# Kernel tuning notes

Measured on AMD Instinct MI355X. Metric: run time of the kernel, lower is better.

## Reference

```python
import jax, jax.numpy as jnp
import numpy as np

B, TIN, E, TOUT, NMEL = 32, 512, 576, 400, 80
PRE, ARNN, DRNN, ADIM, NF, KS = 256, 1024, 1024, 128, 32, 31


def setup_inputs() -> dict:
    key = jax.random.key(0)
    ks = jax.random.split(key, 24)
    r = lambda i, sh, s=0.02: jax.random.normal(ks[i], sh, dtype=jnp.float32) * s
    return {
        'memory': jax.random.normal(ks[0], (B, TIN, E), dtype=jnp.float32) * 0.5,
        'decoder_inputs': jax.random.normal(ks[1], (B, TOUT, NMEL), dtype=jnp.float32) * 0.5,
        'prenet_W1': r(2, (PRE, NMEL)),
        'prenet_W2': r(3, (PRE, PRE)),
        'att_Wih': r(4, (4 * ARNN, PRE + E)),
        'att_Whh': r(5, (4 * ARNN, ARNN)),
        'att_bih': r(6, (4 * ARNN,)),
        'att_bhh': r(7, (4 * ARNN,)),
        'qW': r(8, (ADIM, ARNN)),
        'memW': r(9, (ADIM, E)),
        'convW': r(10, (NF, 2, KS)),
        'convb': r(11, (NF,)),
        'locW': r(12, (ADIM, NF)),
        'vW': r(13, (ADIM,)),
        'dec_Wih': r(14, (4 * DRNN, ARNN + E)),
        'dec_Whh': r(15, (4 * DRNN, DRNN)),
        'dec_bih': r(16, (4 * DRNN,)),
        'dec_bhh': r(17, (4 * DRNN,)),
        'projW': r(18, (NMEL, DRNN + E)),
        'projb': r(19, (NMEL,)),
        'gateW': r(20, (1, DRNN + E)),
        'gateb': r(21, (1,)),
        'memory_lengths': jnp.clip(jax.random.randint(ks[22], (B,), 1, TIN + 1), 16, TIN),
    }


def _lstm(x, h, c, Wih, Whh, bih, bhh):
    g = x @ Wih.T + bih + h @ Whh.T + bhh
    i, f, gg, o = jnp.split(g, 4, axis=-1)  # torch LSTMCell gate order i,f,g,o
    c = jax.nn.sigmoid(f) * c + jax.nn.sigmoid(i) * jnp.tanh(gg)
    h = jax.nn.sigmoid(o) * jnp.tanh(c)
    return h, c


def _forward(memory, decoder_inputs, prenet_W1, prenet_W2, att_Wih, att_Whh, att_bih,
             att_bhh, qW, memW, convW, convb, locW, vW, dec_Wih, dec_Whh, dec_bih,
             dec_bhh, projW, projb, gateW, gateb, memory_lengths):
    b, tin, e = memory.shape
    # go frame + teacher forcing inputs -> prenet (dropout off in deterministic eval)
    go = jnp.zeros((b, 1, NMEL), dtype=memory.dtype)
    di = jnp.concatenate([go, decoder_inputs], axis=1)          # [B, T+1, NMEL]
    x = jax.nn.relu(di @ prenet_W1.T)
    x = jax.nn.relu(x @ prenet_W2.T)                            # [B, T+1, PRE]
    xs = jnp.swapaxes(x, 0, 1)[:-1]                             # [T, B, PRE]
    pmem = memory @ memW.T                                      # [B, TIN, ADIM]
    invalid = jnp.arange(tin)[None, :] >= memory_lengths[:, None]
    pad = KS // 2

    init = (jnp.zeros((b, ARNN)), jnp.zeros((b, ARNN)),
            jnp.zeros((b, DRNN)), jnp.zeros((b, DRNN)),
            jnp.zeros((b, tin)), jnp.zeros((b, tin)),
            jnp.zeros((b, e)))

    def step(carry, xt):
        ah, ac, dh, dc, aw, awc, ctx = carry
        ci = jnp.concatenate([xt, ctx], axis=-1)
        ah, ac = _lstm(ci, ah, ac, att_Wih, att_Whh, att_bih, att_bhh)
        ah = ac  # faithful to source: dropout(attention_cell) overwrites hidden (identity in eval)
        wc = jnp.stack([aw, awc], axis=1)                       # [B, 2, TIN]
        loc = jax.lax.conv_general_dilated(
            wc, convW, (1,), [(pad, pad)],
            dimension_numbers=('NCH', 'OIH', 'NCH')) + convb[None, :, None]
        loc = jnp.swapaxes(loc, 1, 2) @ locW.T                  # [B, TIN, ADIM]
        q = (ah @ qW.T)[:, None, :]                             # [B, 1, ADIM]
        en = jnp.tanh(q + pmem + loc) @ vW                      # [B, TIN]
        en = jnp.where(invalid, -jnp.inf, en)
        aw = jax.nn.softmax(en, axis=1)
        ctx = jnp.einsum('bt,bte->be', aw, memory)
        awc = awc + aw
        d_in = jnp.concatenate([ah, ctx], axis=-1)
        dh, dc = _lstm(d_in, dh, dc, dec_Wih, dec_Whh, dec_bih, dec_bhh)
        dhc = jnp.concatenate([dh, ctx], axis=-1)
        mel = dhc @ projW.T + projb                             # [B, NMEL]
        gate = (dhc @ gateW.T + gateb)[:, 0]                    # [B]
        return (ah, ac, dh, dc, aw, awc, ctx), (mel, gate, aw)

    _, (mels, gates, aligns) = jax.lax.scan(step, init, xs)
    mel_out = jnp.swapaxes(jnp.swapaxes(mels, 0, 1), 1, 2)      # [B, NMEL, T]
    gate_out = jnp.swapaxes(gates, 0, 1)                        # [B, T]
    align_out = jnp.swapaxes(aligns, 0, 1)                      # [B, T, TIN]
    return mel_out, gate_out, align_out


def reference(memory, decoder_inputs, prenet_W1, prenet_W2, att_Wih, att_Whh, att_bih,
              att_bhh, qW, memW, convW, convb, locW, vW, dec_Wih, dec_Whh, dec_bih,
              dec_bhh, projW, projb, gateW, gateb, memory_lengths):
    return _forward(memory, decoder_inputs, prenet_W1, prenet_W2, att_Wih, att_Whh,
                    att_bih, att_bhh, qW, memW, convW, convb, locW, vW, dec_Wih,
                    dec_Whh, dec_bih, dec_bhh, projW, projb, gateW, gateb,
                    memory_lengths)
```

## Files before the change

kernel.cpp:

```cpp
#include <hip/hip_runtime.h>
#include <stdint.h>


#define NB  32
#define TI  512
#define ED  576
#define TO  400
#define NM  80
#define PR  256
#define AR  1024
#define DR  1024
#define AD  128
#define NFl 32
#define KSz 31
#define KA  1856
#define KD  2624
#define NG  4096
#define NKT_A 58
#define NKT_D 82
#define REL_IDX 320
#define MF_OFF  512

#define LDS_WA_BYTES (NKT_A*512*2)
#define LDS_WD_BYTES (NKT_D*512*2)
#define LDS_SCR_FLOATS 4352
#define LDS_TOTAL (LDS_WA_BYTES + LDS_WD_BYTES + LDS_SCR_FLOATS*4)

typedef __attribute__((ext_vector_type(8))) short bf8_t;
typedef __attribute__((ext_vector_type(4))) float f4_t;
typedef __attribute__((ext_vector_type(2))) float f2_t;
typedef unsigned long long ull;

__device__ __forceinline__ short f2bf(float f){
  union { float f; unsigned u; } v; v.f = f;
  unsigned r = v.u + 0x7fffu + ((v.u >> 16) & 1u);
  return (short)(r >> 16);
}
__device__ __forceinline__ float bf2f(short s){
  union { unsigned u; float f; } v; v.u = ((unsigned)(unsigned short)s) << 16; return v.f;
}
__device__ __forceinline__ float sigm(float x){ return 1.f / (1.f + __expf(-x)); }

__device__ __forceinline__ f4_t MFMA(bf8_t a, bf8_t b, f4_t c){
  return __builtin_amdgcn_mfma_f32_16x16x32_bf16(a, b, c, 0, 0, 0);
}

__device__ __forceinline__ float cld(const float* p){
  return __hip_atomic_load(p, __ATOMIC_RELAXED, __HIP_MEMORY_SCOPE_AGENT);
}
__device__ __forceinline__ void cst(float* p, float v){
  __hip_atomic_store(p, v, __ATOMIC_RELAXED, __HIP_MEMORY_SCOPE_AGENT);
}
__device__ __forceinline__ ull cld8(const void* p){
  return __hip_atomic_load((const ull*)p, __ATOMIC_RELAXED, __HIP_MEMORY_SCOPE_AGENT);
}
__device__ __forceinline__ void cst8(void* p, ull v){
  __hip_atomic_store((ull*)p, v, __ATOMIC_RELAXED, __HIP_MEMORY_SCOPE_AGENT);
}
__device__ __forceinline__ bf8_t cld_bf8(const short* p){
  union { bf8_t v; ull q[2]; } u;
  u.q[0] = cld8(p); u.q[1] = cld8(p + 4);
  return u.v;
}
__device__ __forceinline__ void cst_bf8(short* p, bf8_t v){
  union { bf8_t v; ull q[2]; } u; u.v = v;
  cst8(p, u.q[0]); cst8(p + 4, u.q[1]);
}

__device__ __forceinline__ bf8_t packrow(const float* p){
  f4_t a = *(const f4_t*)p;
  f4_t b = *(const f4_t*)(p + 4);
  bf8_t r;
  r[0]=f2bf(a[0]); r[1]=f2bf(a[1]); r[2]=f2bf(a[2]); r[3]=f2bf(a[3]);
  r[4]=f2bf(b[0]); r[5]=f2bf(b[1]); r[6]=f2bf(b[2]); r[7]=f2bf(b[3]);
  return r;
}
__device__ __forceinline__ bf8_t packrow_coh(const float* p){
  union { ull q; float f[2]; } u0, u1, u2, u3;
  u0.q = cld8(p); u1.q = cld8(p + 2); u2.q = cld8(p + 4); u3.q = cld8(p + 6);
  bf8_t r;
  r[0]=f2bf(u0.f[0]); r[1]=f2bf(u0.f[1]);
  r[2]=f2bf(u1.f[0]); r[3]=f2bf(u1.f[1]);
  r[4]=f2bf(u2.f[0]); r[5]=f2bf(u2.f[1]);
  r[6]=f2bf(u3.f[0]); r[7]=f2bf(u3.f[1]);
  return r;
}

struct Par {
  const float *X2, *PMEM;
  const short *WA, *WD, *WQ, *WLOC, *MEMBT, *PJW;
  const float *BSA, *BSD;
  const float *convW, *convb, *vW;
  const float *projb, *gateb;
  const int *mlen;
  float *SBUF, *GATT, *GDEC, *AC, *DH, *DC, *CTX, *AW, *AWC, *EN, *QP;
  short *ABA, *ABD;
  float *out_mel, *out_gate, *out_align;
  unsigned *FLAGS;
};

__device__ __forceinline__ const float* aptr_att(const Par& p, int rp, int t, int b, int k){
  if (k < PR)      return p.X2 + ((size_t)t*NB + b)*PR + k;
  if (k < PR+ED)   return p.CTX + (size_t)rp*NB*ED + b*ED + (k - PR);
  return p.AC + (size_t)rp*NB*AR + b*AR + (k - PR - ED);
}

__device__ __forceinline__ void loadD(const Par& p, int cpar, int ks, int lane,
                                      bf8_t& a0, bf8_t& a1){
  if (ks >= 32 && ks < 50){
    const int kb = ks*32 + ((lane >> 4) << 3);
    const float* c0 = p.CTX + (size_t)cpar*NB*ED + (size_t)(lane & 15)*ED + (kb - AR);
    const float* c1 = p.CTX + (size_t)cpar*NB*ED + (size_t)(16 + (lane & 15))*ED + (kb - AR);
    a0 = packrow_coh(c0);
    a1 = packrow_coh(c1);
  } else {
    a0 = cld_bf8(p.ABD + ((size_t)(0*NKT_D + ks)*64 + lane)*8);
    a1 = cld_bf8(p.ABD + ((size_t)(1*NKT_D + ks)*64 + lane)*8);
  }
}

__device__ __forceinline__ void gbar(unsigned* flags, unsigned tgt){
  __syncthreads();
  if (threadIdx.x == 0)
    __hip_atomic_store(&flags[blockIdx.x], tgt, __ATOMIC_RELAXED, __HIP_MEMORY_SCOPE_AGENT);
  if (blockIdx.x == 0){
    if (threadIdx.x < 256){
      while (__hip_atomic_load(&flags[threadIdx.x], __ATOMIC_RELAXED, __HIP_MEMORY_SCOPE_AGENT) < tgt) {}
    }
    __syncthreads();
    if (threadIdx.x == 0)
      __hip_atomic_store(&flags[REL_IDX], tgt, __ATOMIC_RELAXED, __HIP_MEMORY_SCOPE_AGENT);
  }
  if (threadIdx.x == 0){
    while (__hip_atomic_load(&flags[REL_IDX], __ATOMIC_RELAXED, __HIP_MEMORY_SCOPE_AGENT) < tgt) {}
  }
  __syncthreads();
}

__device__ __forceinline__ void sibbar(unsigned* mf, int bid, int tid, unsigned tgt){
  __syncthreads();
  if (tid == 0)
    __hip_atomic_store(&mf[bid], tgt, __ATOMIC_RELAXED, __HIP_MEMORY_SCOPE_AGENT);
  const int g = (bid >> 3) << 3;
  if (tid < 8){
    while (__hip_atomic_load(&mf[g + tid], __ATOMIC_RELAXED, __HIP_MEMORY_SCOPE_AGENT) < tgt) {}
  }
  __syncthreads();
}

__device__ __forceinline__ void reduce8(float* scr, f4_t& a0, f4_t& a1, int lane, int wv){
  if (wv > 0){
    float* slot = scr + (size_t)((wv - 1)*64 + lane)*8;
    *(f4_t*)slot       = a0;
    *(f4_t*)(slot + 4) = a1;
  }
  __syncthreads();
  if (wv == 0){
    #pragma unroll
    for (int w = 0; w < 7; ++w){
      const float* s2 = scr + (size_t)(w*64 + lane)*8;
      a0 += *(const f4_t*)s2;
      a1 += *(const f4_t*)(s2 + 4);
    }
  }
  __syncthreads();
}

__device__ __forceinline__ void dec_gemm(const Par& p, const short* sWD, float* scr,
                                         int cpar, int bid, int lane, int wv){
  f4_t acc0 = (f4_t){0.f,0.f,0.f,0.f}, acc1 = (f4_t){0.f,0.f,0.f,0.f};
  {
    bf8_t A0[6], A1[6];
    #pragma unroll
    for (int i = 0; i < 6; ++i) loadD(p, cpar, wv + i*8, lane, A0[i], A1[i]);
    #pragma unroll
    for (int i = 0; i < 6; ++i){
      const bf8_t bw = *((const bf8_t*)sWD + (wv + i*8)*64 + lane);
      acc0 = MFMA(A0[i], bw, acc0);
      acc1 = MFMA(A1[i], bw, acc1);
    }
  }
  {
    bf8_t A0[5], A1[5];
    #pragma unroll
    for (int i = 0; i < 5; ++i){
      const int ks = wv + (i + 6)*8;
      if (ks < NKT_D) loadD(p, cpar, ks, lane, A0[i], A1[i]);
    }
    #pragma unroll
    for (int i = 0; i < 5; ++i){
      const int ks = wv + (i + 6)*8;
      if (ks < NKT_D){
        const bf8_t bw = *((const bf8_t*)sWD + ks*64 + lane);
        acc0 = MFMA(A0[i], bw, acc0);
        acc1 = MFMA(A1[i], bw, acc1);
      }
    }
  }
  reduce8(scr, acc0, acc1, lane, wv);
  if (wv == 0){
    const int col = lane & 15, rb2 = (lane >> 4) << 2;
    const int jp = (col & 3)*1024 + bid*4 + (col >> 2);
    const float bs = p.BSD[jp];
    #pragma unroll
    for (int r = 0; r < 4; ++r){
      cst(&p.GDEC[(size_t)(rb2 + r)*NG + jp],      acc0[r] + bs);
      cst(&p.GDEC[(size_t)(16 + rb2 + r)*NG + jp], acc1[r] + bs);
    }
  }
}

__device__ void dec_out(const Par& p, int b, int tprev, int tid, float* sIN){
  const float* ctxg = p.CTX + (size_t)(tprev & 1)*NB*ED + b*ED;
  float cx0 = cld(ctxg + tid);
  float cx1 = (tid < ED - 512) ? cld(ctxg + 512 + tid) : 0.f;
  const int u0 = tid, u1 = tid + 512;
  float g0i = cld(&p.GDEC[b*NG + u0]);
  float g0f = cld(&p.GDEC[b*NG + 1024 + u0]);
  float g0g = cld(&p.GDEC[b*NG + 2048 + u0]);
  float g0o = cld(&p.GDEC[b*NG + 3072 + u0]);
  float g1i = cld(&p.GDEC[b*NG + u1]);
  float g1f = cld(&p.GDEC[b*NG + 1024 + u1]);
  float g1g = cld(&p.GDEC[b*NG + 2048 + u1]);
  float g1o = cld(&p.GDEC[b*NG + 3072 + u1]);
  float dc0 = p.DC[b*DR + u0];
  float dc1 = p.DC[b*DR + u1];
  sIN[1024 + tid] = cx0;
  if (tid < ED - 512) sIN[1024 + 512 + tid] = cx1;
  if (tid < 448) sIN[1600 + tid] = 0.f;
  {
    float c0 = sigm(g0f) * dc0 + sigm(g0i) * tanhf(g0g);
    float c1 = sigm(g1f) * dc1 + sigm(g1i) * tanhf(g1g);
    p.DC[b*DR + u0] = c0;
    p.DC[b*DR + u1] = c1;
    float h0 = sigm(g0o) * tanhf(c0);
    float h1 = sigm(g1o) * tanhf(c1);
    sIN[u0] = h0; sIN[u1] = h1;
    cst(&p.DH[b*DR + u0], h0);
    cst(&p.DH[b*DR + u1], h1);
  }
  __syncthreads();
  const int lane = tid & 63, wv = tid >> 6;
  for (int o = wv; o < 81; o += 8){
    const short* wr = p.PJW + (size_t)o*2048 + lane*8;
    float s = 0.f;
    #pragma unroll
    for (int j = 0; j < 4; ++j){
      const bf8_t w8 = *(const bf8_t*)(wr + j*512);
      const float* v = sIN + j*512 + lane*8;
      s += v[0]*bf2f(w8[0]) + v[1]*bf2f(w8[1]) + v[2]*bf2f(w8[2]) + v[3]*bf2f(w8[3])
         + v[4]*bf2f(w8[4]) + v[5]*bf2f(w8[5]) + v[6]*bf2f(w8[6]) + v[7]*bf2f(w8[7]);
    }
    #pragma unroll
    for (int d = 32; d > 0; d >>= 1) s += __shfl_down(s, d);
    if (lane == 0){
      if (o < 80) p.out_mel[((size_t)b*NM + o)*TO + tprev] = s + p.projb[o];
      else        p.out_gate[(size_t)b*TO + tprev] = s + p.gateb[0];
    }
  }
}

__global__ __launch_bounds__(512) void k_loop(Par p){
  const int bid = blockIdx.x, tid = threadIdx.x;
  const int lane = tid & 63, wv = tid >> 6;

  extern __shared__ char dsm[];
  short* sWA = (short*)dsm;
  short* sWD = (short*)(dsm + LDS_WA_BYTES);
  float* scr = (float*)(dsm + LDS_WA_BYTES + LDS_WD_BYTES);
  unsigned* mf = p.FLAGS + MF_OFF;

  {
    const bf8_t* gwa = (const bf8_t*)(p.WA + (size_t)bid*NKT_A*512);
    bf8_t* lwa = (bf8_t*)sWA;
    for (int i = tid; i < NKT_A*64; i += 512) lwa[i] = gwa[i];
    const bf8_t* gwd = (const bf8_t*)(p.WD + (size_t)bid*NKT_D*512);
    bf8_t* lwd = (bf8_t*)sWD;
    for (int i = tid; i < NKT_D*64; i += 512) lwd[i] = gwd[i];
    __syncthreads();
  }

  for (int t = 0; t < TO; ++t){
    const int wp = t & 1, rp = wp ^ 1;
    const unsigned base = (unsigned)(t * 3);

    {
      f4_t acc0 = (f4_t){0.f,0.f,0.f,0.f}, acc1 = (f4_t){0.f,0.f,0.f,0.f};
      bf8_t A0[8], A1[8];
      #pragma unroll
      for (int i = 0; i < 8; ++i){
        const int ks = wv + i*8;
        if (ks < NKT_A){
          if (t == 0 || (ks >= 8 && ks < 26)){
            const int kb = ks*32 + ((lane >> 4) << 3);
            const float* p0 = aptr_att(p, rp, t, lane & 15, kb);
            const float* p1 = aptr_att(p, rp, t, 16 + (lane & 15), kb);
            if (kb < PR){ A0[i] = packrow(p0);     A1[i] = packrow(p1);     }
            else        { A0[i] = packrow_coh(p0); A1[i] = packrow_coh(p1); }
          } else {
            A0[i] = cld_bf8(p.ABA + ((size_t)(0*NKT_A + ks)*64 + lane)*8);
            A1[i] = cld_bf8(p.ABA + ((size_t)(1*NKT_A + ks)*64 + lane)*8);
          }
        }
      }
      #pragma unroll
      for (int i = 0; i < 8; ++i){
        const int ks = wv + i*8;
        if (ks < NKT_A){
          const bf8_t bw = *((const bf8_t*)sWA + ks*64 + lane);
          acc0 = MFMA(A0[i], bw, acc0);
          acc1 = MFMA(A1[i], bw, acc1);
        }
      }
      reduce8(scr, acc0, acc1, lane, wv);
      if (wv == 0){
        const int col = lane & 15, rb2 = (lane >> 4) << 2;
        const int jp = (col & 3)*1024 + bid*4 + (col >> 2);
        const float bs = p.BSA[jp];
        #pragma unroll
        for (int r = 0; r < 4; ++r){
          cst(&p.GATT[(size_t)(rb2 + r)*NG + jp],      acc0[r] + bs);
          cst(&p.GATT[(size_t)(16 + rb2 + r)*NG + jp], acc1[r] + bs);
        }
      }
      if (t > 0) dec_gemm(p, sWD, scr, rp, bid, lane, wv);
    }
    gbar(p.FLAGS, base + 1);

    {
      if (bid < 32){
        const int nt = bid >> 2, kc = bid & 3;
        short* scrACb = (short*)scr;
        {
          const int u = kc*256 + (tid & 255);
          const int b0 = (tid >> 8) * 16;
          float gi[16], gf[16], gg[16], cp[16];
          #pragma unroll
          for (int j = 0; j < 16; ++j){
            const int b = b0 + j;
            gi[j] = cld(&p.GATT[b*NG + u]);
            gf[j] = cld(&p.GATT[b*NG + 1024 + u]);
            gg[j] = cld(&p.GATT[b*NG + 2048 + u]);
            cp[j] = cld(&p.AC[(size_t)rp*NB*AR + b*AR + u]);
          }
          #pragma unroll
          for (int j = 0; j < 16; ++j){
            const int b = b0 + j;
            float c = sigm(gf[j]) * cp[j] + sigm(gi[j]) * tanhf(gg[j]);
            cst(&p.AC[(size_t)wp*NB*AR + b*AR + u], c);
            scrACb[b*264 + (tid & 255)] = f2bf(c);
          }
        }
        __syncthreads();
        {
          const int kt = kc*8 + wv;
          const int uq = wv*32 + ((lane >> 4) << 3);
          const bf8_t a0 = *(const bf8_t*)(scrACb + (lane & 15)*264 + uq);
          const bf8_t a1 = *(const bf8_t*)(scrACb + (16 + (lane & 15))*264 + uq);
          const bf8_t bw = *(const bf8_t*)(p.WQ + ((size_t)(nt*32 + kt)*64 + lane)*8);
          f4_t q0 = (f4_t){0.f,0.f,0.f,0.f}, q1 = (f4_t){0.f,0.f,0.f,0.f};
          q0 = MFMA(a0, bw, q0);
          q1 = MFMA(a1, bw, q1);
          __syncthreads();
          reduce8(scr, q0, q1, lane, wv);
          if (wv == 0){
            const int col = lane & 15, rb2 = (lane >> 4) << 2;
            float* qp = p.QP + (size_t)kc*NB*AD;
            #pragma unroll
            for (int r = 0; r < 4; ++r){
              cst(&qp[(rb2 + r)*AD + nt*16 + col],      q0[r]);
              cst(&qp[(16 + rb2 + r)*AD + nt*16 + col], q1[r]);
            }
          }
        }
      }
      if (bid >= 224 && t > 0) dec_out(p, bid - 224, t - 1, tid, scr);
      __syncthreads();
      const int b = bid >> 3, tc = bid & 7, t0 = tc*64;
      float* sAWI = scr + 2048;
      short* sCwB = (short*)(scr + 2048 + 192);
      for (int i = tid; i < 94; i += 512){
        int g = t0 - 15 + i;
        float a = 0.f, w = 0.f;
        if (g >= 0 && g < TI){
          a = cld(&p.AW [(size_t)rp*NB*TI + b*TI + g]);
          w = cld(&p.AWC[(size_t)rp*NB*TI + b*TI + g]);
        }
        sAWI[2*i] = a; sAWI[2*i + 1] = w;
      }
      __syncthreads();
      {
        const int wvu = __builtin_amdgcn_readfirstlane(wv);
        const int f0 = wvu * 4;
        float ac4[4];
        #pragma unroll
        for (int ff = 0; ff < 4; ++ff) ac4[ff] = p.convb[f0 + ff];
        for (int k = 0; k < KSz; ++k){
          f2_t a2 = *(const f2_t*)&sAWI[2*(lane + k)];
          #pragma unroll
          for (int ff = 0; ff < 4; ++ff){
            ac4[ff] += a2[0] * p.convW[((f0+ff)*2 + 0)*KSz + k]
                     + a2[1] * p.convW[((f0+ff)*2 + 1)*KSz + k];
          }
        }
        #pragma unroll
        for (int ff = 0; ff < 4; ++ff) sCwB[lane*40 + f0 + ff] = f2bf(ac4[ff]);
      }
      __syncthreads();
      {
        for (int j = wv; j < 32; j += 8){
          const int mt = j >> 3, nt2 = j & 7;
          const bf8_t afr = *(const bf8_t*)(sCwB + (mt*16 + (lane & 15))*40 + ((lane >> 4) << 3));
          const bf8_t bfr = *(const bf8_t*)(p.WLOC + (size_t)(nt2*64 + lane)*8);
          f4_t c = (f4_t){0.f,0.f,0.f,0.f};
          c = MFMA(afr, bfr, c);
          const int tl2 = mt*16 + ((lane >> 4) << 2);
          const int d2  = nt2*16 + (lane & 15);
          #pragma unroll
          for (int r = 0; r < 4; ++r){
            const int tg2 = t0 + tl2 + r;
            p.SBUF[((size_t)b*TI + tg2)*AD + d2] =
              c[r] + p.PMEM[((size_t)b*TI + tg2)*AD + d2];
          }
        }
      }
    }
    gbar(p.FLAGS, base + 2);

    {
      float* sQ = scr;
      if (tid < 128){
        const int b = bid >> 3;
        sQ[tid] = cld(&p.QP[(size_t)b*AD + tid])
                + cld(&p.QP[(size_t)NB*AD + b*AD + tid])
                + cld(&p.QP[(size_t)2*NB*AD + b*AD + tid])
                + cld(&p.QP[(size_t)3*NB*AD + b*AD + tid]);
      }
      if (wv == 0 && bid < 208){
        const int r = lane & 15, koff = (lane >> 4) << 3;
        if (bid < 80){
          if (t < TO - 1){
            const int m = bid / 40, idx = bid % 40;
            const int ks = (idx < 8) ? idx : idx + 18;
            const int row = m*16 + r;
            const int k = ks*32 + koff;
            bf8_t v = (k < PR)
              ? packrow(p.X2 + ((size_t)(t+1)*NB + row)*PR + k)
              : packrow_coh(p.AC + (size_t)wp*NB*AR + (size_t)row*AR + (k - PR - ED));
            cst_bf8(p.ABA + ((size_t)(m*NKT_A + ks)*64 + lane)*8, v);
          }
        } else {
          const int j2 = bid - 80;
          const int m = j2 / 64, idx = j2 % 64;
          const int ks = (idx < 32) ? idx : idx + 18;
          const int row = m*16 + r;
          const int k = ks*32 + koff;
          bf8_t v = (k < AR)
            ? packrow_coh(p.AC + (size_t)wp*NB*AR + (size_t)row*AR + k)
            : packrow_coh(p.DH + (size_t)row*DR + (k - AR - ED));
          cst_bf8(p.ABD + ((size_t)(m*NKT_D + ks)*64 + lane)*8, v);
        }
      }
      __syncthreads();
      const int b = bid >> 3, tc = bid & 7;
      const int tl = tid >> 3, dq = tid & 7;
      const int tg = tc*64 + tl;
      const float* sb = p.SBUF + ((size_t)b*TI + tg)*AD;
      float s = 0.f;
      #pragma unroll
      for (int j = 0; j < 16; ++j){
        const int d = dq*16 + j;
        s += p.vW[d] * tanhf(sQ[d] + sb[d]);
      }
      s += __shfl_down(s, 1);
      s += __shfl_down(s, 2);
      s += __shfl_down(s, 4);
      if (dq == 0)
        cst(&p.EN[b*TI + tg], (tg < p.mlen[b]) ? s : -1e30f);
    }
    sibbar(mf, bid, tid, (unsigned)(t + 1));

    {
      const int b = bid >> 3, ec = bid & 7;
      float* red = scr;
      float* sp  = scr + 64;
      const float e = cld(&p.EN[b*TI + tid]);
      float m = e;
      #pragma unroll
      for (int d = 32; d > 0; d >>= 1) m = fmaxf(m, __shfl_xor(m, d));
      if (lane == 0) red[wv] = m;
      __syncthreads();
      const float M = fmaxf(fmaxf(fmaxf(red[0], red[1]), fmaxf(red[2], red[3])),
                            fmaxf(fmaxf(red[4], red[5]), fmaxf(red[6], red[7])));
      const float x = __expf(e - M);
      float z = x;
      #pragma unroll
      for (int d = 32; d > 0; d >>= 1) z += __shfl_xor(z, d);
      __syncthreads();
      if (lane == 0) red[wv] = z;
      __syncthreads();
      const float Z = red[0]+red[1]+red[2]+red[3]+red[4]+red[5]+red[6]+red[7];
      const float pv = x / Z;
      sp[tid] = pv;
      __syncthreads();
      if (ec == 0){
        cst(&p.AW [(size_t)wp*NB*TI + b*TI + tid], pv);
        cst(&p.AWC[(size_t)wp*NB*TI + b*TI + tid],
            cld(&p.AWC[(size_t)rp*NB*TI + b*TI + tid]) + pv);
        p.out_align[((size_t)b*TO + t)*TI + tid] = pv;
      }
      #pragma unroll
      for (int ii = 0; ii < 9; ++ii){
        const int e2 = ec*72 + wv*9 + ii;
        const short* row = p.MEMBT + ((size_t)b*ED + e2)*TI;
        const bf8_t w8 = *(const bf8_t*)(row + lane*8);
        const float* v = sp + lane*8;
        float a2 = v[0]*bf2f(w8[0]) + v[1]*bf2f(w8[1]) + v[2]*bf2f(w8[2]) + v[3]*bf2f(w8[3])
                 + v[4]*bf2f(w8[4]) + v[5]*bf2f(w8[5]) + v[6]*bf2f(w8[6]) + v[7]*bf2f(w8[7]);
        #pragma unroll
        for (int d = 32; d > 0; d >>= 1) a2 += __shfl_down(a2, d);
        if (lane == 0)
          cst(&p.CTX[(size_t)wp*NB*ED + b*ED + e2], a2);
      }
    }
    gbar(p.FLAGS, base + 3);
  }

  dec_gemm(p, sWD, scr, (TO - 1) & 1, bid, lane, wv);
  gbar(p.FLAGS, (unsigned)(TO*3 + 1));
  if (bid >= 224) dec_out(p, bid - 224, TO - 1, tid, scr);
}

__global__ __launch_bounds__(256) void k_init(float* z, int nz,
                                              float* bsa, const float* a1, const float* a2,
                                              float* bsd, const float* d1, const float* d2){
  const int idx = blockIdx.x*256 + threadIdx.x, st = gridDim.x*256;
  for (int i = idx; i < nz; i += st) z[i] = 0.f;
  for (int i = idx; i < NG; i += st){ bsa[i] = a1[i] + a2[i]; bsd[i] = d1[i] + d2[i]; }
}

__global__ __launch_bounds__(256) void k_prenet1(const float* di, const float* W1, float* X1){
  const int t = blockIdx.x, tid = threadIdx.x;
  __shared__ float sdi[NB*NM];
  for (int i = tid; i < NB*NM; i += 256){
    const int b = i / NM, k = i - b*NM;
    sdi[i] = (t == 0) ? 0.f : di[((size_t)b*TO + (t-1))*NM + k];
  }
  __syncthreads();
  float acc[NB];
  #pragma unroll
  for (int b = 0; b < NB; ++b) acc[b] = 0.f;
  const int j = tid;
  for (int k = 0; k < NM; ++k){
    const float w = W1[j*NM + k];
    #pragma unroll
    for (int b = 0; b < NB; ++b) acc[b] += sdi[b*NM + k] * w;
  }
  for (int b = 0; b < NB; ++b)
    X1[((size_t)t*NB + b)*PR + j] = fmaxf(acc[b], 0.f);
}

__global__ __launch_bounds__(256) void k_prenet2(const float* X1, const float* W2, float* X2){
  const int t = blockIdx.x, tid = threadIdx.x;
  __shared__ float sx[NB*PR];
  for (int i = tid; i < NB*PR; i += 256) sx[i] = X1[(size_t)t*NB*PR + i];
  __syncthreads();
  float acc[NB];
  #pragma unroll
  for (int b = 0; b < NB; ++b) acc[b] = 0.f;
  const int j = tid;
  for (int k = 0; k < PR; ++k){
    const float w = W2[j*PR + k];
    #pragma unroll
    for (int b = 0; b < NB; ++b) acc[b] += sx[b*PR + k] * w;
  }
  for (int b = 0; b < NB; ++b)
    X2[((size_t)t*NB + b)*PR + j] = fmaxf(acc[b], 0.f);
}

__global__ __launch_bounds__(256) void k_pmem(const float* mem, const float* memW, float* pm){
  const int b = blockIdx.x >> 3, tc = blockIdx.x & 7, tid = threadIdx.x;
  __shared__ float sW[64*AD];
  __shared__ float sM[64*65];
  const int tl = tid >> 2, dq = tid & 3;
  float acc[32];
  #pragma unroll
  for (int i = 0; i < 32; ++i) acc[i] = 0.f;
  for (int kc = 0; kc < 9; ++kc){
    __syncthreads();
    for (int i = tid; i < 64*AD; i += 256){
      const int d = i >> 6, kl = i & 63;
      sW[kl*AD + ((d + kl) & 127)] = memW[(size_t)d*ED + kc*64 + kl];
    }
    for (int i = tid; i < 64*64; i += 256){
      const int tt = i >> 6, kl = i & 63;
      sM[tt*65 + kl] = mem[((size_t)b*TI + tc*64 + tt)*ED + kc*64 + kl];
    }
    __syncthreads();
    for (int kl = 0; kl < 64; ++kl){
      const float mv = sM[tl*65 + kl];
      #pragma unroll
      for (int d2 = 0; d2 < 32; ++d2)
        acc[d2] += mv * sW[kl*AD + ((dq*32 + d2 + kl) & 127)];
    }
  }
  for (int d2 = 0; d2 < 32; ++d2)
    pm[((size_t)b*TI + tc*64 + tl)*AD + dq*32 + d2] = acc[d2];
}

__global__ __launch_bounds__(256) void k_membt(const float* mem, short* mt){
  const int b = blockIdx.x / 36, ec = blockIdx.x % 36;
  __shared__ float sT[64*17];
  for (int tc = 0; tc < 8; ++tc){
    __syncthreads();
    for (int i = threadIdx.x; i < 64*16; i += 256){
      const int tt = i >> 4, e = i & 15;
      sT[tt*17 + e] = mem[((size_t)b*TI + tc*64 + tt)*ED + ec*16 + e];
    }
    __syncthreads();
    for (int i = threadIdx.x; i < 16*64; i += 256){
      const int e = i >> 6, tt = i & 63;
      mt[((size_t)b*ED + ec*16 + e)*TI + tc*64 + tt] = f2bf(sT[tt*17 + e]);
    }
  }
}

__global__ __launch_bounds__(64) void k_swz_gate(const float* Wih, const float* Whh,
                                                 short* dst, int split, int nkt){
  const int bidx = blockIdx.x;
  const int nt = bidx / nkt, kt = bidx - nt*nkt;
  const int lane = threadIdx.x;
  const int nl = lane & 15;
  const int jp = (nl & 3)*1024 + nt*4 + (nl >> 2);
  const int k0 = kt*32 + ((lane >> 4) << 3);
  bf8_t v;
  #pragma unroll
  for (int jj = 0; jj < 8; ++jj){
    const int k = k0 + jj;
    const float f = (k < split) ? Wih[(size_t)jp*split + k]
                                : Whh[(size_t)jp*1024 + (k - split)];
    v[jj] = f2bf(f);
  }
  *(bf8_t*)(dst + (size_t)bidx*512 + lane*8) = v;
}

__global__ __launch_bounds__(64) void k_swz_q(const float* qW, short* dst){
  const int bidx = blockIdx.x;
  const int nt = bidx >> 5, kt = bidx & 31;
  const int lane = threadIdx.x;
  const int d = nt*16 + (lane & 15);
  const int k0 = kt*32 + ((lane >> 4) << 3);
  bf8_t v;
  #pragma unroll
  for (int jj = 0; jj < 8; ++jj) v[jj] = f2bf(qW[(size_t)d*AR + k0 + jj]);
  *(bf8_t*)(dst + (size_t)bidx*512 + lane*8) = v;
}

__global__ __launch_bounds__(64) void k_swz_loc(const float* locW, short* dst){
  const int nt = blockIdx.x;
  const int lane = threadIdx.x;
  const int d = nt*16 + (lane & 15);
  const int f0 = (lane >> 4) << 3;
  bf8_t v;
  #pragma unroll
  for (int jj = 0; jj < 8; ++jj) v[jj] = f2bf(locW[d*NFl + f0 + jj]);
  *(bf8_t*)(dst + (size_t)(nt*64 + lane)*8) = v;
}

__global__ __launch_bounds__(256) void k_swz_proj(const float* projW, const float* gateW,
                                                  short* dst){
  const int o = blockIdx.x;
  const float* src = (o < 80) ? (projW + (size_t)o*1600) : gateW;
  for (int k = threadIdx.x; k < 2048; k += 256)
    dst[(size_t)o*2048 + k] = (k < 1600) ? f2bf(src[k]) : (short)0;
}

extern "C" void kernel_launch(void* const* d_in, const int* in_sizes, int n_in,
                              void* d_out, int out_size, void* d_ws, size_t ws_size,
                              hipStream_t stream){
  const float* mem    = (const float*)d_in[0];
  const float* dec_in = (const float*)d_in[1];
  const float* pW1    = (const float*)d_in[2];
  const float* pW2    = (const float*)d_in[3];
  const float* aWih   = (const float*)d_in[4];
  const float* aWhh   = (const float*)d_in[5];
  const float* aBih   = (const float*)d_in[6];
  const float* aBhh   = (const float*)d_in[7];
  const float* qW     = (const float*)d_in[8];
  const float* memW   = (const float*)d_in[9];
  const float* convW  = (const float*)d_in[10];
  const float* convb  = (const float*)d_in[11];
  const float* locW   = (const float*)d_in[12];
  const float* vW     = (const float*)d_in[13];
  const float* dWih   = (const float*)d_in[14];
  const float* dWhh   = (const float*)d_in[15];
  const float* dBih   = (const float*)d_in[16];
  const float* dBhh   = (const float*)d_in[17];
  const float* projW  = (const float*)d_in[18];
  const float* projb  = (const float*)d_in[19];
  const float* gateW  = (const float*)d_in[20];
  const float* gateb  = (const float*)d_in[21];
  const int*   mlen   = (const int*)d_in[22];
  (void)in_sizes; (void)n_in; (void)out_size; (void)ws_size;

  char* basep = (char*)d_ws;
  size_t off = 0;
  auto carve = [&](size_t bytes) -> char* {
    char* r = basep + off;
    off = (off + bytes + 255) & ~(size_t)255;
    return r;
  };
  short* WA    = (short*)carve((size_t)NG*KA*2);
  short* WD    = (short*)carve((size_t)NG*KD*2);
  short* WQ    = (short*)carve((size_t)AD*AR*2);
  short* WLOC  = (short*)carve((size_t)AD*NFl*2);
  short* MEMBT = (short*)carve((size_t)NB*TI*ED*2);
  short* PJW   = (short*)carve((size_t)81*2048*2);
  float* X1    = (float*)carve((size_t)TO*NB*PR*4);
  float* X2    = (float*)carve((size_t)TO*NB*PR*4);
  float* PMEM  = (float*)carve((size_t)NB*TI*AD*4);
  float* SBUF  = (float*)carve((size_t)NB*TI*AD*4);
  float* GATT  = (float*)carve((size_t)NB*NG*4);
  float* GDEC  = (float*)carve((size_t)NB*NG*4);
  float* BSA   = (float*)carve((size_t)NG*4);
  float* BSD   = (float*)carve((size_t)NG*4);
  short* ABA   = (short*)carve((size_t)2*NKT_A*512*2);
  short* ABD   = (short*)carve((size_t)2*NKT_D*512*2);
  float* AC    = (float*)carve((size_t)2*NB*AR*4);
  float* DH    = (float*)carve((size_t)NB*DR*4);
  float* DC    = (float*)carve((size_t)NB*DR*4);
  float* CTX   = (float*)carve((size_t)2*NB*ED*4);
  float* AW    = (float*)carve((size_t)2*NB*TI*4);
  float* AWC   = (float*)carve((size_t)2*NB*TI*4);
  float* EN    = (float*)carve((size_t)NB*TI*4);
  float* QP    = (float*)carve((size_t)4*NB*AD*4);
  unsigned* FLAGS = (unsigned*)carve(4096);
  const int nz = (int)((((char*)FLAGS + 4096) - (char*)AC) / 4);

  float* out_mel   = (float*)d_out;
  float* out_gate  = out_mel + (size_t)NB*NM*TO;
  float* out_align = out_gate + (size_t)NB*TO;

  k_init   <<<dim3(512), dim3(256), 0, stream>>>(AC, nz, BSA, aBih, aBhh, BSD, dBih, dBhh);
  k_prenet1<<<dim3(TO),  dim3(256), 0, stream>>>(dec_in, pW1, X1);
  k_prenet2<<<dim3(TO),  dim3(256), 0, stream>>>(X1, pW2, X2);
  k_pmem   <<<dim3(256), dim3(256), 0, stream>>>(mem, memW, PMEM);
  k_membt  <<<dim3(NB*36), dim3(256), 0, stream>>>(mem, MEMBT);
  k_swz_gate<<<dim3(256*NKT_A), dim3(64), 0, stream>>>(aWih, aWhh, WA, 832, NKT_A);
  k_swz_gate<<<dim3(256*NKT_D), dim3(64), 0, stream>>>(dWih, dWhh, WD, 1600, NKT_D);
  k_swz_q  <<<dim3(256), dim3(64), 0, stream>>>(qW, WQ);
  k_swz_loc<<<dim3(8),   dim3(64), 0, stream>>>(locW, WLOC);
  k_swz_proj<<<dim3(81), dim3(256), 0, stream>>>(projW, gateW, PJW);

  Par p;
  p.X2 = X2; p.PMEM = PMEM;
  p.WA = WA; p.WD = WD; p.WQ = WQ; p.WLOC = WLOC; p.MEMBT = MEMBT; p.PJW = PJW;
  p.BSA = BSA; p.BSD = BSD;
  p.convW = convW; p.convb = convb; p.vW = vW;
  p.projb = projb; p.gateb = gateb;
  p.mlen = mlen;
  p.SBUF = SBUF; p.GATT = GATT; p.GDEC = GDEC;
  p.AC = AC; p.DH = DH; p.DC = DC; p.CTX = CTX;
  p.AW = AW; p.AWC = AWC; p.EN = EN; p.QP = QP;
  p.ABA = ABA; p.ABD = ABD;
  p.out_mel = out_mel; p.out_gate = out_gate; p.out_align = out_align;
  p.FLAGS = FLAGS;

  (void)hipFuncSetAttribute((const void*)k_loop,
                            hipFuncAttributeMaxDynamicSharedMemorySize, LDS_TOTAL);
  k_loop<<<dim3(256), dim3(512), LDS_TOTAL, stream>>>(p);
}
```

Measured before the change: 35.17 ms.

## Fuse LSTM cell updates into gate GEMM blocks and keep cell state in LDS

Each block now applies the LSTM cell nonlinearity right after its own gate GEMM, holding cell state for its four units in LDS. This removes the GATT/GDEC global round-trips and the separate 32-block cell-update phase. The location-conv MFMA is moved into the energy phase and fused with the tanh/v reduction, which removes the SBUF global buffer. The stage schedule across grid barriers is reorganized, AC is single-buffered, and the query projection now reads AC straight from global.

```diff
diff --git a/kernel.cpp b/kernel.cpp
--- a/kernel.cpp
+++ b/kernel.cpp
@@ -15,15 +15,18 @@
 #define KSz 31
 #define KA  1856
 #define KD  2624
-#define NG  4096
 #define NKT_A 58
 #define NKT_D 82
 #define REL_IDX 320
 #define MF_OFF  512
 
+#define SCR_CWB 3584
+#define SCR_ACC 4608
+#define SCR_DCC 4736
+#define SCR_SQ  4864
 #define LDS_WA_BYTES (NKT_A*512*2)
 #define LDS_WD_BYTES (NKT_D*512*2)
-#define LDS_SCR_FLOATS 4352
+#define LDS_SCR_FLOATS 4992
 #define LDS_TOTAL (LDS_WA_BYTES + LDS_WD_BYTES + LDS_SCR_FLOATS*4)
 
 typedef __attribute__((ext_vector_type(8))) short bf8_t;
@@ -93,7 +96,7 @@
   const float *convW, *convb, *vW;
   const float *projb, *gateb;
   const int *mlen;
-  float *SBUF, *GATT, *GDEC, *AC, *DH, *DC, *CTX, *AW, *AWC, *EN, *QP;
+  float *AC, *DH, *CTX, *AW, *AWC, *EN, *QP;
   short *ABA, *ABD;
   float *out_mel, *out_gate, *out_align;
   unsigned *FLAGS;
@@ -102,7 +105,7 @@
 __device__ __forceinline__ const float* aptr_att(const Par& p, int rp, int t, int b, int k){
   if (k < PR)      return p.X2 + ((size_t)t*NB + b)*PR + k;
   if (k < PR+ED)   return p.CTX + (size_t)rp*NB*ED + b*ED + (k - PR);
-  return p.AC + (size_t)rp*NB*AR + b*AR + (k - PR - ED);
+  return p.AC + (size_t)b*AR + (k - PR - ED);
 }
 
 __device__ __forceinline__ void loadD(const Par& p, int cpar, int ks, int lane,
@@ -166,8 +169,9 @@
   __syncthreads();
 }
 
-__device__ __forceinline__ void dec_gemm(const Par& p, const short* sWD, float* scr,
-                                         int cpar, int bid, int lane, int wv){
+__device__ __forceinline__ void dec_gates_cell(const Par& p, const short* sWD, float* scr,
+                                               float* sDCc, int cpar, int bid,
+                                               int lane, int wv, int tid){
   f4_t acc0 = (f4_t){0.f,0.f,0.f,0.f}, acc1 = (f4_t){0.f,0.f,0.f,0.f};
   {
     bf8_t A0[6], A1[6];
@@ -198,47 +202,41 @@
     }
   }
   reduce8(scr, acc0, acc1, lane, wv);
+  float* sG = scr;
   if (wv == 0){
     const int col = lane & 15, rb2 = (lane >> 4) << 2;
     const int jp = (col & 3)*1024 + bid*4 + (col >> 2);
     const float bs = p.BSD[jp];
     #pragma unroll
     for (int r = 0; r < 4; ++r){
-      cst(&p.GDEC[(size_t)(rb2 + r)*NG + jp],      acc0[r] + bs);
-      cst(&p.GDEC[(size_t)(16 + rb2 + r)*NG + jp], acc1[r] + bs);
-    }
-  }
-}
-
-__device__ void dec_out(const Par& p, int b, int tprev, int tid, float* sIN){
+      sG[(rb2 + r)*16 + col]      = acc0[r] + bs;
+      sG[(16 + rb2 + r)*16 + col] = acc1[r] + bs;
+    }
+  }
+  __syncthreads();
+  if (tid < 128){
+    const int b = tid >> 2, ul = tid & 3;
+    const float gi = sG[b*16 + ul*4 + 0];
+    const float gf = sG[b*16 + ul*4 + 1];
+    const float gg = sG[b*16 + ul*4 + 2];
+    const float go = sG[b*16 + ul*4 + 3];
+    const float c  = sigm(gf) * sDCc[tid] + sigm(gi) * tanhf(gg);
+    sDCc[tid] = c;
+    cst(&p.DH[(size_t)b*DR + bid*4 + ul], sigm(go) * tanhf(c));
+  }
+  __syncthreads();
+}
+
+__device__ void dec_proj(const Par& p, int b, int tprev, int tid, float* sIN){
   const float* ctxg = p.CTX + (size_t)(tprev & 1)*NB*ED + b*ED;
+  float h0  = cld(&p.DH[(size_t)b*DR + tid]);
+  float h1  = cld(&p.DH[(size_t)b*DR + 512 + tid]);
   float cx0 = cld(ctxg + tid);
   float cx1 = (tid < ED - 512) ? cld(ctxg + 512 + tid) : 0.f;
-  const int u0 = tid, u1 = tid + 512;
-  float g0i = cld(&p.GDEC[b*NG + u0]);
-  float g0f = cld(&p.GDEC[b*NG + 1024 + u0]);
-  float g0g = cld(&p.GDEC[b*NG + 2048 + u0]);
-  float g0o = cld(&p.GDEC[b*NG + 3072 + u0]);
-  float g1i = cld(&p.GDEC[b*NG + u1]);
-  float g1f = cld(&p.GDEC[b*NG + 1024 + u1]);
-  float g1g = cld(&p.GDEC[b*NG + 2048 + u1]);
-  float g1o = cld(&p.GDEC[b*NG + 3072 + u1]);
-  float dc0 = p.DC[b*DR + u0];
-  float dc1 = p.DC[b*DR + u1];
+  sIN[tid] = h0; sIN[512 + tid] = h1;
   sIN[1024 + tid] = cx0;
-  if (tid < ED - 512) sIN[1024 + 512 + tid] = cx1;
+  if (tid < ED - 512) sIN[1536 + tid] = cx1;
   if (tid < 448) sIN[1600 + tid] = 0.f;
-  {
-    float c0 = sigm(g0f) * dc0 + sigm(g0i) * tanhf(g0g);
-    float c1 = sigm(g1f) * dc1 + sigm(g1i) * tanhf(g1g);
-    p.DC[b*DR + u0] = c0;
-    p.DC[b*DR + u1] = c1;
-    float h0 = sigm(g0o) * tanhf(c0);
-    float h1 = sigm(g1o) * tanhf(c1);
-    sIN[u0] = h0; sIN[u1] = h1;
-    cst(&p.DH[b*DR + u0], h0);
-    cst(&p.DH[b*DR + u1], h1);
-  }
   __syncthreads();
   const int lane = tid & 63, wv = tid >> 6;
   for (int o = wv; o < 81; o += 8){
@@ -258,6 +256,7 @@
       else        p.out_gate[(size_t)b*TO + tprev] = s + p.gateb[0];
     }
   }
+  __syncthreads();
 }
 
 __global__ __launch_bounds__(512) void k_loop(Par p){
@@ -268,9 +267,12 @@
   short* sWA = (short*)dsm;
   short* sWD = (short*)(dsm + LDS_WA_BYTES);
   float* scr = (float*)(dsm + LDS_WA_BYTES + LDS_WD_BYTES);
+  float* sACc = scr + SCR_ACC;
+  float* sDCc = scr + SCR_DCC;
   unsigned* mf = p.FLAGS + MF_OFF;
 
   {
+    if (tid < 128){ sACc[tid] = 0.f; sDCc[tid] = 0.f; }
     const bf8_t* gwa = (const bf8_t*)(p.WA + (size_t)bid*NKT_A*512);
     bf8_t* lwa = (bf8_t*)sWA;
     for (int i = tid; i < NKT_A*64; i += 512) lwa[i] = gwa[i];
@@ -313,72 +315,32 @@
         }
       }
       reduce8(scr, acc0, acc1, lane, wv);
+      float* sG = scr;
       if (wv == 0){
         const int col = lane & 15, rb2 = (lane >> 4) << 2;
         const int jp = (col & 3)*1024 + bid*4 + (col >> 2);
         const float bs = p.BSA[jp];
         #pragma unroll
         for (int r = 0; r < 4; ++r){
-          cst(&p.GATT[(size_t)(rb2 + r)*NG + jp],      acc0[r] + bs);
-          cst(&p.GATT[(size_t)(16 + rb2 + r)*NG + jp], acc1[r] + bs);
+          sG[(rb2 + r)*16 + col]      = acc0[r] + bs;
+          sG[(16 + rb2 + r)*16 + col] = acc1[r] + bs;
         }
       }
-      if (t > 0) dec_gemm(p, sWD, scr, rp, bid, lane, wv);
-    }
-    gbar(p.FLAGS, base + 1);
-
-    {
-      if (bid < 32){
-        const int nt = bid >> 2, kc = bid & 3;
-        short* scrACb = (short*)scr;
-        {
-          const int u = kc*256 + (tid & 255);
-          const int b0 = (tid >> 8) * 16;
-          float gi[16], gf[16], gg[16], cp[16];
-          #pragma unroll
-          for (int j = 0; j < 16; ++j){
-            const int b = b0 + j;
-            gi[j] = cld(&p.GATT[b*NG + u]);
-            gf[j] = cld(&p.GATT[b*NG + 1024 + u]);
-            gg[j] = cld(&p.GATT[b*NG + 2048 + u]);
-            cp[j] = cld(&p.AC[(size_t)rp*NB*AR + b*AR + u]);
-          }
-          #pragma unroll
-          for (int j = 0; j < 16; ++j){
-            const int b = b0 + j;
-            float c = sigm(gf[j]) * cp[j] + sigm(gi[j]) * tanhf(gg[j]);
-            cst(&p.AC[(size_t)wp*NB*AR + b*AR + u], c);
-            scrACb[b*264 + (tid & 255)] = f2bf(c);
-          }
-        }
-        __syncthreads();
-        {
-          const int kt = kc*8 + wv;
-          const int uq = wv*32 + ((lane >> 4) << 3);
-          const bf8_t a0 = *(const bf8_t*)(scrACb + (lane & 15)*264 + uq);
-          const bf8_t a1 = *(const bf8_t*)(scrACb + (16 + (lane & 15))*264 + uq);
-          const bf8_t bw = *(const bf8_t*)(p.WQ + ((size_t)(nt*32 + kt)*64 + lane)*8);
-          f4_t q0 = (f4_t){0.f,0.f,0.f,0.f}, q1 = (f4_t){0.f,0.f,0.f,0.f};
-          q0 = MFMA(a0, bw, q0);
-          q1 = MFMA(a1, bw, q1);
-          __syncthreads();
-          reduce8(scr, q0, q1, lane, wv);
-          if (wv == 0){
-            const int col = lane & 15, rb2 = (lane >> 4) << 2;
-            float* qp = p.QP + (size_t)kc*NB*AD;
-            #pragma unroll
-            for (int r = 0; r < 4; ++r){
-              cst(&qp[(rb2 + r)*AD + nt*16 + col],      q0[r]);
-              cst(&qp[(16 + rb2 + r)*AD + nt*16 + col], q1[r]);
-            }
-          }
-        }
-      }
-      if (bid >= 224 && t > 0) dec_out(p, bid - 224, t - 1, tid, scr);
-      __syncthreads();
+      __syncthreads();
+      if (tid < 128){
+        const int b = tid >> 2, ul = tid & 3;
+        const float gi = sG[b*16 + ul*4 + 0];
+        const float gf = sG[b*16 + ul*4 + 1];
+        const float gg = sG[b*16 + ul*4 + 2];
+        const float c  = sigm(gf) * sACc[tid] + sigm(gi) * tanhf(gg);
+        sACc[tid] = c;
+        cst(&p.AC[(size_t)b*AR + bid*4 + ul], c);
+      }
+      __syncthreads();
+      if (t > 0) dec_gates_cell(p, sWD, scr, sDCc, rp, bid, lane, wv, tid);
       const int b = bid >> 3, tc = bid & 7, t0 = tc*64;
-      float* sAWI = scr + 2048;
-      short* sCwB = (short*)(scr + 2048 + 192);
+      float* sAWI = scr;
+      short* sCwB = (short*)(scr + SCR_CWB);
       for (int i = tid; i < 94; i += 512){
         int g = t0 - 15 + i;
         float a = 0.f, w = 0.f;
@@ -404,31 +366,39 @@
           }
         }
         #pragma unroll
-        for (int ff = 0; ff < 4; ++ff) sCwB[lane*40 + f0 + ff] = f2bf(ac4[ff]);
-      }
-      __syncthreads();
-      {
-        for (int j = wv; j < 32; j += 8){
-          const int mt = j >> 3, nt2 = j & 7;
-          const bf8_t afr = *(const bf8_t*)(sCwB + (mt*16 + (lane & 15))*40 + ((lane >> 4) << 3));
-          const bf8_t bfr = *(const bf8_t*)(p.WLOC + (size_t)(nt2*64 + lane)*8);
-          f4_t c = (f4_t){0.f,0.f,0.f,0.f};
-          c = MFMA(afr, bfr, c);
-          const int tl2 = mt*16 + ((lane >> 4) << 2);
-          const int d2  = nt2*16 + (lane & 15);
+        for (int ff = 0; ff < 4; ++ff) sCwB[lane*32 + f0 + ff] = f2bf(ac4[ff]);
+      }
+    }
+    gbar(p.FLAGS, base + 1);
+
+    {
+      if (bid < 32){
+        const int nt = bid >> 2, kc = bid & 3;
+        const int kt = kc*8 + wv;
+        const int kb = kt*32 + ((lane >> 4) << 3);
+        bf8_t a0 = packrow_coh(p.AC + (size_t)(lane & 15)*AR + kb);
+        bf8_t a1 = packrow_coh(p.AC + (size_t)(16 + (lane & 15))*AR + kb);
+        const bf8_t bw = *(const bf8_t*)(p.WQ + ((size_t)(nt*32 + kt)*64 + lane)*8);
+        f4_t q0 = (f4_t){0.f,0.f,0.f,0.f}, q1 = (f4_t){0.f,0.f,0.f,0.f};
+        q0 = MFMA(a0, bw, q0);
+        q1 = MFMA(a1, bw, q1);
+        reduce8(scr, q0, q1, lane, wv);
+        if (wv == 0){
+          const int col = lane & 15, rb2 = (lane >> 4) << 2;
+          float* qp = p.QP + (size_t)kc*NB*AD;
           #pragma unroll
           for (int r = 0; r < 4; ++r){
-            const int tg2 = t0 + tl2 + r;
-            p.SBUF[((size_t)b*TI + tg2)*AD + d2] =
-              c[r] + p.PMEM[((size_t)b*TI + tg2)*AD + d2];
+            cst(&qp[(rb2 + r)*AD + nt*16 + col],      q0[r]);
+            cst(&qp[(16 + rb2 + r)*AD + nt*16 + col], q1[r]);
           }
         }
       }
+      if (bid >= 224 && t > 0) dec_proj(p, bid - 224, t - 1, tid, scr);
     }
     gbar(p.FLAGS, base + 2);
 
     {
-      float* sQ = scr;
+      float* sQ = scr + SCR_SQ;
       if (tid < 128){
         const int b = bid >> 3;
         sQ[tid] = cld(&p.QP[(size_t)b*AD + tid])
@@ -446,7 +416,7 @@
             const int k = ks*32 + koff;
             bf8_t v = (k < PR)
               ? packrow(p.X2 + ((size_t)(t+1)*NB + row)*PR + k)
-              : packrow_coh(p.AC + (size_t)wp*NB*AR + (size_t)row*AR + (k - PR - ED));
+              : packrow_coh(p.AC + (size_t)row*AR + (k - PR - ED));
             cst_bf8(p.ABA + ((size_t)(m*NKT_A + ks)*64 + lane)*8, v);
           }
         } else {
@@ -456,27 +426,45 @@
           const int row = m*16 + r;
           const int k = ks*32 + koff;
           bf8_t v = (k < AR)
-            ? packrow_coh(p.AC + (size_t)wp*NB*AR + (size_t)row*AR + k)
+            ? packrow_coh(p.AC + (size_t)row*AR + k)
             : packrow_coh(p.DH + (size_t)row*DR + (k - AR - ED));
           cst_bf8(p.ABD + ((size_t)(m*NKT_D + ks)*64 + lane)*8, v);
         }
       }
       __syncthreads();
-      const int b = bid >> 3, tc = bid & 7;
-      const int tl = tid >> 3, dq = tid & 7;
-      const int tg = tc*64 + tl;
-      const float* sb = p.SBUF + ((size_t)b*TI + tg)*AD;
-      float s = 0.f;
+      const int b = bid >> 3, tc = bid & 7, t0 = tc*64;
+      short* sCwB = (short*)(scr + SCR_CWB);
+      float* eP = scr;
+      const int g = lane >> 4, li = lane & 15;
+      const int d2 = wv*16 + li;
+      const float vw = p.vW[d2];
+      const float qd = sQ[d2];
+      const bf8_t bfr = *(const bf8_t*)(p.WLOC + (size_t)(wv*64 + lane)*8);
       #pragma unroll
-      for (int j = 0; j < 16; ++j){
-        const int d = dq*16 + j;
-        s += p.vW[d] * tanhf(sQ[d] + sb[d]);
-      }
-      s += __shfl_down(s, 1);
-      s += __shfl_down(s, 2);
-      s += __shfl_down(s, 4);
-      if (dq == 0)
-        cst(&p.EN[b*TI + tg], (tg < p.mlen[b]) ? s : -1e30f);
+      for (int mt = 0; mt < 4; ++mt){
+        const bf8_t afr = *(const bf8_t*)(sCwB + (mt*16 + li)*32 + (g << 3));
+        f4_t c = (f4_t){0.f,0.f,0.f,0.f};
+        c = MFMA(afr, bfr, c);
+        #pragma unroll
+        for (int r = 0; r < 4; ++r){
+          const int tg = t0 + mt*16 + g*4 + r;
+          const float val = c[r] + p.PMEM[((size_t)b*TI + tg)*AD + d2];
+          float v = vw * tanhf(qd + val);
+          v += __shfl_xor(v, 1);
+          v += __shfl_xor(v, 2);
+          v += __shfl_xor(v, 4);
+          v += __shfl_xor(v, 8);
+          if (li == 0) eP[wv*64 + mt*16 + g*4 + r] = v;
+        }
+      }
+      __syncthreads();
+      if (tid < 64){
+        float e = eP[tid];
+        #pragma unroll
+        for (int w2 = 1; w2 < 8; ++w2) e += eP[w2*64 + tid];
+        const int tg = t0 + tid;
+        cst(&p.EN[b*TI + tg], (tg < p.mlen[b]) ? e : -1e30f);
+      }
     }
     sibbar(mf, bid, tid, (unsigned)(t + 1));
 
@@ -526,15 +514,16 @@
     gbar(p.FLAGS, base + 3);
   }
 
-  dec_gemm(p, sWD, scr, (TO - 1) & 1, bid, lane, wv);
+  dec_gates_cell(p, sWD, scr, sDCc, (TO - 1) & 1, bid, lane, wv, tid);
   gbar(p.FLAGS, (unsigned)(TO*3 + 1));
-  if (bid >= 224) dec_out(p, bid - 224, TO - 1, tid, scr);
+  if (bid >= 224) dec_proj(p, bid - 224, TO - 1, tid, scr);
 }
 
 __global__ __launch_bounds__(256) void k_init(float* z, int nz,
                                               float* bsa, const float* a1, const float* a2,
                                               float* bsd, const float* d1, const float* d2){
   const int idx = blockIdx.x*256 + threadIdx.x, st = gridDim.x*256;
+  const int NG = 4096;
   for (int i = idx; i < nz; i += st) z[i] = 0.f;
   for (int i = idx; i < NG; i += st){ bsa[i] = a1[i] + a2[i]; bsd[i] = d1[i] + d2[i]; }
 }
@@ -710,6 +699,7 @@
     off = (off + bytes + 255) & ~(size_t)255;
     return r;
   };
+  const int NG = 4096;
   short* WA    = (short*)carve((size_t)NG*KA*2);
   short* WD    = (short*)carve((size_t)NG*KD*2);
   short* WQ    = (short*)carve((size_t)AD*AR*2);
@@ -719,16 +709,12 @@
   float* X1    = (float*)carve((size_t)TO*NB*PR*4);
   float* X2    = (float*)carve((size_t)TO*NB*PR*4);
   float* PMEM  = (float*)carve((size_t)NB*TI*AD*4);
-  float* SBUF  = (float*)carve((size_t)NB*TI*AD*4);
-  float* GATT  = (float*)carve((size_t)NB*NG*4);
-  float* GDEC  = (float*)carve((size_t)NB*NG*4);
   float* BSA   = (float*)carve((size_t)NG*4);
   float* BSD   = (float*)carve((size_t)NG*4);
   short* ABA   = (short*)carve((size_t)2*NKT_A*512*2);
   short* ABD   = (short*)carve((size_t)2*NKT_D*512*2);
-  float* AC    = (float*)carve((size_t)2*NB*AR*4);
+  float* AC    = (float*)carve((size_t)NB*AR*4);
   float* DH    = (float*)carve((size_t)NB*DR*4);
-  float* DC    = (float*)carve((size_t)NB*DR*4);
   float* CTX   = (float*)carve((size_t)2*NB*ED*4);
   float* AW    = (float*)carve((size_t)2*NB*TI*4);
   float* AWC   = (float*)carve((size_t)2*NB*TI*4);
@@ -759,8 +745,7 @@
   p.convW = convW; p.convb = convb; p.vW = vW;
   p.projb = projb; p.gateb = gateb;
   p.mlen = mlen;
-  p.SBUF = SBUF; p.GATT = GATT; p.GDEC = GDEC;
-  p.AC = AC; p.DH = DH; p.DC = DC; p.CTX = CTX;
+  p.AC = AC; p.DH = DH; p.CTX = CTX;
   p.AW = AW; p.AWC = AWC; p.EN = EN; p.QP = QP;
   p.ABA = ABA; p.ABD = ABD;
   p.out_mel = out_mel; p.out_gate = out_gate; p.out_align = out_align;
```

Result: faster. 32.43 ms (-7.8%).
